# Performance work log

Measured on AMD Instinct MI355X. Metric: run time of the kernel, lower is better.

## Reference

```python
import jax, jax.numpy as jnp
import numpy as np

ALPHA = 0.2  # LeakyReLU negative slope


def setup_inputs() -> dict:
    key = jax.random.key(0)
    k1, k2, k3, k4 = jax.random.split(key, 4)
    B, N, F_IN, F_OUT = 4, 4096, 256, 256
    h = jax.random.normal(k1, (B, N, F_IN), dtype=jnp.float32)
    adj = jax.random.randint(k2, (B, N, N), 0, 2, dtype=jnp.int32)
    # xavier_normal with gain=1.414: std = gain*sqrt(2/(fan_in+fan_out))
    std_W = 1.414 * np.sqrt(2.0 / (F_IN + F_OUT))
    W = jax.random.normal(k3, (F_IN, F_OUT), dtype=jnp.float32) * std_W
    std_a = 1.414 * np.sqrt(2.0 / (1 + 2 * F_OUT))
    a = jax.random.normal(k4, (1, 2 * F_OUT), dtype=jnp.float32) * std_a
    return {"h": h, "adj": adj, "W": W, "a": a}


def reference(h, adj, W, a):
    # h: [B, N, F_in], adj: [B, N, N] (0/1), W: [F_in, F_out], a: [1, 2*F_out]
    F_out = W.shape[1]
    Hh = jnp.einsum('bni,io->bno', h, W)               # [B, N, F_out]
    a_src = a[0, :F_out]                                # attends to edge source i
    a_dst = a[0, F_out:]                                # attends to edge target j
    s = jnp.einsum('bno,o->bn', Hh, a_src)              # [B, N]
    d = jnp.einsum('bno,o->bn', Hh, a_dst)              # [B, N]
    # score(i,j) = a . concat(Hh_i, Hh_j) = s_i + d_j
    logits = s[:, :, None] + d[:, None, :]              # [B, N, N]
    # edge_e = exp(-leakyrelu(score)) only on edges (adj nonzero), else 0
    e = jnp.where(adj != 0,
                  jnp.exp(-jax.nn.leaky_relu(logits, negative_slope=ALPHA)),
                  jnp.zeros((), dtype=Hh.dtype))        # [B, N, N]
    rowsum = jnp.sum(e, axis=-1, keepdims=True)         # [B, N, 1]
    # rows with zero sum keep divisor 1 (as in the torch code)
    rowsum = jnp.where(rowsum == 0.0, 1.0, rowsum)
    h_prime = jnp.einsum('bnm,bmo->bno', e, Hh) / rowsum  # [B, N, F_out]
    return jax.nn.elu(h_prime)  # concat=True branch
```

## Files before the change

kernel.cpp:

```cpp
#include <hip/hip_runtime.h>

#define LRELU_ALPHA 0.2f

typedef __bf16 bf16x8 __attribute__((ext_vector_type(8)));
typedef unsigned short u16;
typedef unsigned short u16x8 __attribute__((ext_vector_type(8)));
typedef float f32x4 __attribute__((ext_vector_type(4)));
typedef int int4v __attribute__((ext_vector_type(4)));
typedef unsigned int u32;
typedef unsigned int u32x4 __attribute__((ext_vector_type(4)));
typedef unsigned long long u64;

__device__ __forceinline__ u16 f2bf(float f) {
  unsigned int u = __float_as_uint(f);
  u += 0x7fffu + ((u >> 16) & 1u);
  return (u16)(u >> 16);
}

__global__ __launch_bounds__(256) void packw(const int* __restrict__ adj,
                                             u32* __restrict__ maskg,
                                             const float* __restrict__ W,
                                             u16* __restrict__ WbT) {
  const int tid = threadIdx.x;
  if (blockIdx.x >= 4096) {
    int idx = (blockIdx.x - 4096) * 256 + tid;
    WbT[idx] = f2bf(W[(idx & 255) * 256 + (idx >> 8)]);
    return;
  }
  const int l = tid & 63, w = tid >> 6;
  const size_t row = (size_t)blockIdx.x * 4 + w;
  const int* arow = adj + row * 4096;
  u64* mrow = (u64*)(maskg + row * 128);
  for (int it = 0; it < 16; ++it) {
    const int* base = arow + it * 256;
    int v0 = base[l], v1 = base[l + 64], v2 = base[l + 128], v3 = base[l + 192];
    u64 b0 = __ballot(v0 != 0);
    u64 b1 = __ballot(v1 != 0);
    u64 b2 = __ballot(v2 != 0);
    u64 b3 = __ballot(v3 != 0);
    if (l == 0) {
      mrow[it * 4 + 0] = b0;
      mrow[it * 4 + 1] = b1;
      mrow[it * 4 + 2] = b2;
      mrow[it * 4 + 3] = b3;
    }
  }
}

__global__ __launch_bounds__(256) void gemm1(const float* __restrict__ h,
                                             const u16* __restrict__ WbT,
                                             const float* __restrict__ a,
                                             u16* __restrict__ HhTt,
                                             float* __restrict__ sbuf,
                                             float* __restrict__ dbuf) {
  const int tid = threadIdx.x, bid = blockIdx.x;
  const int l = tid & 63, w = tid >> 6;
  const int lr = l & 15;
  const int lk = (l >> 4) << 3;
  const int rowA = bid * 64 + 16 * w + lr;
  const float* hrow = h + (size_t)rowA * 256 + lk;

  f32x4 acc[16];
#pragma unroll
  for (int n = 0; n < 16; ++n) acc[n] = (f32x4){0.f, 0.f, 0.f, 0.f};

  for (int k0 = 0; k0 < 256; k0 += 32) {
    f32x4 a0 = *(const f32x4*)(hrow + k0);
    f32x4 a1 = *(const f32x4*)(hrow + k0 + 4);
    u16x8 au;
    au[0] = f2bf(a0[0]); au[1] = f2bf(a0[1]); au[2] = f2bf(a0[2]); au[3] = f2bf(a0[3]);
    au[4] = f2bf(a1[0]); au[5] = f2bf(a1[1]); au[6] = f2bf(a1[2]); au[7] = f2bf(a1[3]);
    bf16x8 af = __builtin_bit_cast(bf16x8, au);
#pragma unroll
    for (int n = 0; n < 16; ++n) {
      int4v bv = *(const int4v*)(WbT + (size_t)(16 * n + lr) * 256 + k0 + lk);
      bf16x8 bf = __builtin_bit_cast(bf16x8, bv);
      acc[n] = __builtin_amdgcn_mfma_f32_16x16x32_bf16(af, bf, acc[n], 0, 0, 0);
    }
  }

  float sp[4] = {0.f, 0.f, 0.f, 0.f}, dp[4] = {0.f, 0.f, 0.f, 0.f};
#pragma unroll
  for (int n = 0; n < 16; ++n) {
    int col = 16 * n + lr;
    float as = a[col];
    float ad = a[256 + col];
#pragma unroll
    for (int rr = 0; rr < 4; ++rr) {
      int row = bid * 64 + 16 * w + ((l >> 4) << 2) + rr;
      int bb = row >> 12, kk = row & 4095;
      float v = acc[n][rr];
      size_t addr = (size_t)bb * 1048576 + (size_t)(kk >> 5) * 8192 +
                    (col >> 4) * 512 + ((kk >> 3) & 3) * 128 + (col & 15) * 8 +
                    (kk & 7);
      HhTt[addr] = f2bf(v);
      sp[rr] += v * as;
      dp[rr] += v * ad;
    }
  }
#pragma unroll
  for (int rr = 0; rr < 4; ++rr) {
#pragma unroll
    for (int off = 1; off < 16; off <<= 1) {
      sp[rr] += __shfl_xor(sp[rr], off);
      dp[rr] += __shfl_xor(dp[rr], off);
    }
  }
  if ((l & 15) == 0) {
#pragma unroll
    for (int rr = 0; rr < 4; ++rr) {
      int row = bid * 64 + 16 * w + ((l >> 4) << 2) + rr;
      sbuf[row] = sp[rr];
      dbuf[row] = dp[rr];
    }
  }
}

__global__ __launch_bounds__(256, 2) void gat_main(const u32* __restrict__ maskg,
                                                   const u16* __restrict__ HhTt,
                                                   const float* __restrict__ s,
                                                   const float* __restrict__ d,
                                                   float* __restrict__ out) {
  __shared__ __align__(16) u32 Mk[32 * 128];
  __shared__ __align__(16) float Dl[4096];

  const int tid = threadIdx.x, bid = blockIdx.x;
  const int xcd = bid & 7;
  const int t = (xcd << 6) | (bid >> 3);
  const int b = t >> 7;
  const int rowbase = (t & 127) << 5;

  const int l = tid & 63, w = tid >> 6;
  const int lr = l & 15, lkg = l >> 4;
  const int wr = w & 1, wc = w >> 1;
  const int rowl = wr * 16 + lr;

  for (int i = tid; i < 1024; i += 256)
    *(f32x4*)&Dl[i * 4] = *(const f32x4*)(d + b * 4096 + i * 4);
  {
    const u32* mrow = maskg + ((size_t)(b * 4096 + rowbase)) * 128;
    const int r = tid >> 3, c0 = (tid & 7) * 16;
#pragma unroll
    for (int j = 0; j < 16; ++j) {
      int c = c0 + j;
      Mk[r * 128 + ((c + r) & 127)] = mrow[r * 128 + c];
    }
  }
  const float s_row = s[b * 4096 + rowbase + rowl];
  __syncthreads();

  const char* bsrc = (const char*)HhTt +
      ((size_t)b * 1048576 + (wc * 8) * 512 + lkg * 128 + lr * 8) * 2;

  f32x4 acc[8];
#pragma unroll
  for (int n = 0; n < 8; ++n) acc[n] = (f32x4){0.f, 0.f, 0.f, 0.f};
  float racc = 0.f;
  const int mkbase = rowl * 128;

  for (int step = 0; step < 128; ++step) {
    const char* bs = bsrc + (size_t)step * 16384;
    int4v bv[8];
#pragma unroll
    for (int n = 0; n < 8; ++n) bv[n] = *(const int4v*)(bs + n * 1024);

    u32 mword = Mk[mkbase + ((step + rowl) & 127)];
    u32 m8 = mword >> (lkg * 8);
    f32x4 dA = *(const f32x4*)&Dl[step * 32 + lkg * 8];
    f32x4 dB = *(const f32x4*)&Dl[step * 32 + lkg * 8 + 4];
    float ev[8];
#pragma unroll
    for (int j = 0; j < 8; ++j) {
      float lg = s_row + (j < 4 ? dA[j & 3] : dB[j & 3]);
      float tt = fmaxf(lg, LRELU_ALPHA * lg);
      float e = ((m8 >> j) & 1) ? __expf(-tt) : 0.f;
      racc += e;
      ev[j] = e;
    }
    u32x4 pk;
    asm("v_cvt_pk_bf16_f32 %0, %1, %2" : "=v"(pk[0]) : "v"(ev[0]), "v"(ev[1]));
    asm("v_cvt_pk_bf16_f32 %0, %1, %2" : "=v"(pk[1]) : "v"(ev[2]), "v"(ev[3]));
    asm("v_cvt_pk_bf16_f32 %0, %1, %2" : "=v"(pk[2]) : "v"(ev[4]), "v"(ev[5]));
    asm("v_cvt_pk_bf16_f32 %0, %1, %2" : "=v"(pk[3]) : "v"(ev[6]), "v"(ev[7]));
    bf16x8 af = __builtin_bit_cast(bf16x8, pk);

#pragma unroll
    for (int n = 0; n < 8; ++n) {
      bf16x8 bfv = __builtin_bit_cast(bf16x8, bv[n]);
      acc[n] = __builtin_amdgcn_mfma_f32_16x16x32_bf16(af, bfv, acc[n], 0, 0, 0);
    }
  }

  racc += __shfl_xor(racc, 16);
  racc += __shfl_xor(racc, 32);
  float inv[4];
#pragma unroll
  for (int reg = 0; reg < 4; ++reg) {
    float rsv = __shfl(racc, lkg * 4 + reg);
    inv[reg] = 1.f / (rsv == 0.f ? 1.f : rsv);
  }

  const size_t obase =
      ((size_t)(b * 4096 + rowbase + wr * 16 + lkg * 4)) * 256 + wc * 128;
#pragma unroll
  for (int n = 0; n < 8; ++n) {
#pragma unroll
    for (int reg = 0; reg < 4; ++reg) {
      float v = acc[n][reg] * inv[reg];
      out[obase + (size_t)reg * 256 + 16 * n + lr] =
          v > 0.f ? v : (__expf(v) - 1.f);
    }
  }
}

extern "C" void kernel_launch(void* const* d_in, const int* in_sizes, int n_in,
                              void* d_out, int out_size, void* d_ws, size_t ws_size,
                              hipStream_t stream) {
  const float* h = (const float*)d_in[0];
  const int* adj = (const int*)d_in[1];
  const float* W = (const float*)d_in[2];
  const float* a = (const float*)d_in[3];
  float* out = (float*)d_out;

  u16* WbT   = (u16*)d_ws;
  u16* HhTt  = (u16*)((char*)d_ws + 131072);
  float* sb  = (float*)((char*)d_ws + 131072 + 8388608);
  float* db  = sb + 16384;
  u32* maskg = (u32*)((char*)d_ws + 131072 + 8388608 + 131072);

  hipLaunchKernelGGL(packw,    dim3(4352), dim3(256), 0, stream, adj, maskg, W, WbT);
  hipLaunchKernelGGL(gemm1,    dim3(256),  dim3(256), 0, stream, h, WbT, a, HhTt, sb, db);
  hipLaunchKernelGGL(gat_main, dim3(512),  dim3(256), 0, stream, maskg, HhTt, sb, db, out);
}
```

Measured before the change: 172.0 us.

## Split gat_main output columns across blocks, double-buffer loads, raise MFMA priority

Reorganises gat_main into 512-thread blocks that each cover 64 rows and half of the output features, giving every wave 4 MFMA tiles instead of 8. The step loop is software-pipelined with two register buffers, so the next step's B-fragment, mask word and d values are loaded while the current step computes. The MFMA group is wrapped in s_setprio to raise its issue priority. In exchange, each row's exp/mask work is now recomputed by four waves instead of two. The launch bound of 512 threads with 4 blocks caps registers tightly and may cause spills, and LDS per block grows to 48KB, which limits how many blocks fit on a CU.

```diff
diff --git a/kernel.cpp b/kernel.cpp
--- a/kernel.cpp
+++ b/kernel.cpp
@@ -116,26 +116,28 @@
   }
 }
 
-__global__ __launch_bounds__(256, 2) void gat_main(const u32* __restrict__ maskg,
+__global__ __launch_bounds__(512, 4) void gat_main(const u32* __restrict__ maskg,
                                                    const u16* __restrict__ HhTt,
                                                    const float* __restrict__ s,
                                                    const float* __restrict__ d,
                                                    float* __restrict__ out) {
-  __shared__ __align__(16) u32 Mk[32 * 128];
+  __shared__ __align__(16) u32 Mk[64 * 128];
   __shared__ __align__(16) float Dl[4096];
 
   const int tid = threadIdx.x, bid = blockIdx.x;
   const int xcd = bid & 7;
   const int t = (xcd << 6) | (bid >> 3);
   const int b = t >> 7;
-  const int rowbase = (t & 127) << 5;
+  const int loc = t & 127;
+  const int rowbase = (loc >> 1) << 6;
+  const int ch = loc & 1;
 
   const int l = tid & 63, w = tid >> 6;
   const int lr = l & 15, lkg = l >> 4;
-  const int wr = w & 1, wc = w >> 1;
+  const int wr = w & 3, wc = w >> 2;
   const int rowl = wr * 16 + lr;
 
-  for (int i = tid; i < 1024; i += 256)
+  for (int i = tid; i < 1024; i += 512)
     *(f32x4*)&Dl[i * 4] = *(const f32x4*)(d + b * 4096 + i * 4);
   {
     const u32* mrow = maskg + ((size_t)(b * 4096 + rowbase)) * 128;
@@ -150,46 +152,70 @@
   __syncthreads();
 
   const char* bsrc = (const char*)HhTt +
-      ((size_t)b * 1048576 + (wc * 8) * 512 + lkg * 128 + lr * 8) * 2;
-
-  f32x4 acc[8];
-#pragma unroll
-  for (int n = 0; n < 8; ++n) acc[n] = (f32x4){0.f, 0.f, 0.f, 0.f};
+      ((size_t)b * 1048576 + (size_t)(ch * 8 + wc * 4) * 512 + lkg * 128 + lr * 8) * 2;
+
+  f32x4 acc[4];
+#pragma unroll
+  for (int n = 0; n < 4; ++n) acc[n] = (f32x4){0.f, 0.f, 0.f, 0.f};
   float racc = 0.f;
   const int mkbase = rowl * 128;
 
-  for (int step = 0; step < 128; ++step) {
-    const char* bs = bsrc + (size_t)step * 16384;
-    int4v bv[8];
-#pragma unroll
-    for (int n = 0; n < 8; ++n) bv[n] = *(const int4v*)(bs + n * 1024);
-
-    u32 mword = Mk[mkbase + ((step + rowl) & 127)];
-    u32 m8 = mword >> (lkg * 8);
-    f32x4 dA = *(const f32x4*)&Dl[step * 32 + lkg * 8];
-    f32x4 dB = *(const f32x4*)&Dl[step * 32 + lkg * 8 + 4];
-    float ev[8];
-#pragma unroll
-    for (int j = 0; j < 8; ++j) {
-      float lg = s_row + (j < 4 ? dA[j & 3] : dB[j & 3]);
-      float tt = fmaxf(lg, LRELU_ALPHA * lg);
-      float e = ((m8 >> j) & 1) ? __expf(-tt) : 0.f;
-      racc += e;
-      ev[j] = e;
-    }
-    u32x4 pk;
-    asm("v_cvt_pk_bf16_f32 %0, %1, %2" : "=v"(pk[0]) : "v"(ev[0]), "v"(ev[1]));
-    asm("v_cvt_pk_bf16_f32 %0, %1, %2" : "=v"(pk[1]) : "v"(ev[2]), "v"(ev[3]));
-    asm("v_cvt_pk_bf16_f32 %0, %1, %2" : "=v"(pk[2]) : "v"(ev[4]), "v"(ev[5]));
-    asm("v_cvt_pk_bf16_f32 %0, %1, %2" : "=v"(pk[3]) : "v"(ev[6]), "v"(ev[7]));
-    bf16x8 af = __builtin_bit_cast(bf16x8, pk);
-
-#pragma unroll
-    for (int n = 0; n < 8; ++n) {
-      bf16x8 bfv = __builtin_bit_cast(bf16x8, bv[n]);
-      acc[n] = __builtin_amdgcn_mfma_f32_16x16x32_bf16(af, bfv, acc[n], 0, 0, 0);
-    }
-  }
+  int4v bvA0, bvA1, bvA2, bvA3, bvB0, bvB1, bvB2, bvB3;
+  u32 mwA, mwB;
+  f32x4 dA0, dA1, dB0, dB1;
+
+#define LOADSTEP(S, STEP)                                                     \
+  {                                                                           \
+    const int st_ = (STEP) & 127;                                             \
+    const char* bs_ = bsrc + (size_t)st_ * 16384;                             \
+    bv##S##0 = *(const int4v*)(bs_);                                          \
+    bv##S##1 = *(const int4v*)(bs_ + 1024);                                   \
+    bv##S##2 = *(const int4v*)(bs_ + 2048);                                   \
+    bv##S##3 = *(const int4v*)(bs_ + 3072);                                   \
+    mw##S = Mk[mkbase + ((st_ + rowl) & 127)];                                \
+    d##S##0 = *(const f32x4*)&Dl[st_ * 32 + lkg * 8];                         \
+    d##S##1 = *(const f32x4*)&Dl[st_ * 32 + lkg * 8 + 4];                     \
+  }
+
+#define COMP(S)                                                               \
+  {                                                                           \
+    u32 m8 = mw##S >> (lkg * 8);                                              \
+    float ev[8];                                                              \
+    _Pragma("unroll")                                                         \
+    for (int j = 0; j < 8; ++j) {                                             \
+      float lg = s_row + (j < 4 ? d##S##0[j & 3] : d##S##1[j & 3]);           \
+      float tt = fmaxf(lg, LRELU_ALPHA * lg);                                 \
+      float e = ((m8 >> j) & 1) ? __expf(-tt) : 0.f;                          \
+      racc += e;                                                              \
+      ev[j] = e;                                                              \
+    }                                                                         \
+    u32x4 pk;                                                                 \
+    asm("v_cvt_pk_bf16_f32 %0, %1, %2" : "=v"(pk[0]) : "v"(ev[0]), "v"(ev[1])); \
+    asm("v_cvt_pk_bf16_f32 %0, %1, %2" : "=v"(pk[1]) : "v"(ev[2]), "v"(ev[3])); \
+    asm("v_cvt_pk_bf16_f32 %0, %1, %2" : "=v"(pk[2]) : "v"(ev[4]), "v"(ev[5])); \
+    asm("v_cvt_pk_bf16_f32 %0, %1, %2" : "=v"(pk[3]) : "v"(ev[6]), "v"(ev[7])); \
+    bf16x8 af = __builtin_bit_cast(bf16x8, pk);                               \
+    __builtin_amdgcn_s_setprio(1);                                            \
+    acc[0] = __builtin_amdgcn_mfma_f32_16x16x32_bf16(                         \
+        af, __builtin_bit_cast(bf16x8, bv##S##0), acc[0], 0, 0, 0);           \
+    acc[1] = __builtin_amdgcn_mfma_f32_16x16x32_bf16(                         \
+        af, __builtin_bit_cast(bf16x8, bv##S##1), acc[1], 0, 0, 0);           \
+    acc[2] = __builtin_amdgcn_mfma_f32_16x16x32_bf16(                         \
+        af, __builtin_bit_cast(bf16x8, bv##S##2), acc[2], 0, 0, 0);           \
+    acc[3] = __builtin_amdgcn_mfma_f32_16x16x32_bf16(                         \
+        af, __builtin_bit_cast(bf16x8, bv##S##3), acc[3], 0, 0, 0);           \
+    __builtin_amdgcn_s_setprio(0);                                            \
+  }
+
+  LOADSTEP(A, 0)
+  for (int st = 0; st < 128; st += 2) {
+    LOADSTEP(B, st + 1)
+    COMP(A)
+    LOADSTEP(A, st + 2)
+    COMP(B)
+  }
+#undef LOADSTEP
+#undef COMP
 
   racc += __shfl_xor(racc, 16);
   racc += __shfl_xor(racc, 32);
@@ -201,9 +227,9 @@
   }
 
   const size_t obase =
-      ((size_t)(b * 4096 + rowbase + wr * 16 + lkg * 4)) * 256 + wc * 128;
-#pragma unroll
-  for (int n = 0; n < 8; ++n) {
+      ((size_t)(b * 4096 + rowbase + wr * 16 + lkg * 4)) * 256 + ch * 128 + wc * 64;
+#pragma unroll
+  for (int n = 0; n < 4; ++n) {
 #pragma unroll
     for (int reg = 0; reg < 4; ++reg) {
       float v = acc[n][reg] * inv[reg];
@@ -230,5 +256,5 @@
 
   hipLaunchKernelGGL(packw,    dim3(4352), dim3(256), 0, stream, adj, maskg, W, WbT);
   hipLaunchKernelGGL(gemm1,    dim3(256),  dim3(256), 0, stream, h, WbT, a, HhTt, sb, db);
-  hipLaunchKernelGGL(gat_main, dim3(512),  dim3(256), 0, stream, maskg, HhTt, sb, db, out);
-}
+  hipLaunchKernelGGL(gat_main, dim3(512),  dim3(512), 0, stream, maskg, HhTt, sb, db, out);
+}
```

Result: slower. 176.1 us (+2.4%).

## Fuse adjacency bit-packing into main kernel and switch to 32x32 MFMA tiles

Applied to the files above, without the earlier changes.

Removes the separate packing pass that wrote a bitmask to global memory. The main attention kernel now reads the int32 adjacency directly and ballots it into a shared-memory bitmask per block. Blocks grow to 512 threads covering 64 rows each, and the inner loop uses 32x32x16 bf16 MFMAs with a matching new Hh layout and s_setprio around the MFMA group. This avoids a global round trip for the mask and improves MFMA reuse, but adjacency reads are no longer overlapped with other work and the block count halves.

```diff
diff --git a/kernel.cpp b/kernel.cpp
--- a/kernel.cpp
+++ b/kernel.cpp
@@ -6,6 +6,7 @@
 typedef unsigned short u16;
 typedef unsigned short u16x8 __attribute__((ext_vector_type(8)));
 typedef float f32x4 __attribute__((ext_vector_type(4)));
+typedef float f32x16 __attribute__((ext_vector_type(16)));
 typedef int int4v __attribute__((ext_vector_type(4)));
 typedef unsigned int u32;
 typedef unsigned int u32x4 __attribute__((ext_vector_type(4)));
@@ -17,34 +18,10 @@
   return (u16)(u >> 16);
 }
 
-__global__ __launch_bounds__(256) void packw(const int* __restrict__ adj,
-                                             u32* __restrict__ maskg,
-                                             const float* __restrict__ W,
+__global__ __launch_bounds__(256) void wcast(const float* __restrict__ W,
                                              u16* __restrict__ WbT) {
-  const int tid = threadIdx.x;
-  if (blockIdx.x >= 4096) {
-    int idx = (blockIdx.x - 4096) * 256 + tid;
-    WbT[idx] = f2bf(W[(idx & 255) * 256 + (idx >> 8)]);
-    return;
-  }
-  const int l = tid & 63, w = tid >> 6;
-  const size_t row = (size_t)blockIdx.x * 4 + w;
-  const int* arow = adj + row * 4096;
-  u64* mrow = (u64*)(maskg + row * 128);
-  for (int it = 0; it < 16; ++it) {
-    const int* base = arow + it * 256;
-    int v0 = base[l], v1 = base[l + 64], v2 = base[l + 128], v3 = base[l + 192];
-    u64 b0 = __ballot(v0 != 0);
-    u64 b1 = __ballot(v1 != 0);
-    u64 b2 = __ballot(v2 != 0);
-    u64 b3 = __ballot(v3 != 0);
-    if (l == 0) {
-      mrow[it * 4 + 0] = b0;
-      mrow[it * 4 + 1] = b1;
-      mrow[it * 4 + 2] = b2;
-      mrow[it * 4 + 3] = b3;
-    }
-  }
+  int idx = blockIdx.x * 256 + threadIdx.x;
+  WbT[idx] = f2bf(W[(idx & 255) * 256 + (idx >> 8)]);
 }
 
 __global__ __launch_bounds__(256) void gemm1(const float* __restrict__ h,
@@ -90,9 +67,8 @@
       int row = bid * 64 + 16 * w + ((l >> 4) << 2) + rr;
       int bb = row >> 12, kk = row & 4095;
       float v = acc[n][rr];
-      size_t addr = (size_t)bb * 1048576 + (size_t)(kk >> 5) * 8192 +
-                    (col >> 4) * 512 + ((kk >> 3) & 3) * 128 + (col & 15) * 8 +
-                    (kk & 7);
+      size_t addr = (size_t)bb * 1048576 + (size_t)(kk >> 4) * 4096 +
+                    (col >> 5) * 512 + (col & 31) * 16 + (kk & 15);
       HhTt[addr] = f2bf(v);
       sp[rr] += v * as;
       dp[rr] += v * ad;
@@ -116,100 +92,125 @@
   }
 }
 
-__global__ __launch_bounds__(256, 2) void gat_main(const u32* __restrict__ maskg,
-                                                   const u16* __restrict__ HhTt,
-                                                   const float* __restrict__ s,
-                                                   const float* __restrict__ d,
-                                                   float* __restrict__ out) {
-  __shared__ __align__(16) u32 Mk[32 * 128];
+__global__ __launch_bounds__(512, 2) void gat_fused(const int* __restrict__ adj,
+                                                    const u16* __restrict__ HhTt,
+                                                    const float* __restrict__ s,
+                                                    const float* __restrict__ d,
+                                                    float* __restrict__ out) {
+  __shared__ __align__(16) u32 Mk[64 * 128];
   __shared__ __align__(16) float Dl[4096];
 
   const int tid = threadIdx.x, bid = blockIdx.x;
   const int xcd = bid & 7;
-  const int t = (xcd << 6) | (bid >> 3);
-  const int b = t >> 7;
-  const int rowbase = (t & 127) << 5;
+  const int t = (xcd << 5) | (bid >> 3);
+  const int b = t >> 6;
+  const int rowbase = (t & 63) << 6;
 
   const int l = tid & 63, w = tid >> 6;
-  const int lr = l & 15, lkg = l >> 4;
   const int wr = w & 1, wc = w >> 1;
-  const int rowl = wr * 16 + lr;
-
-  for (int i = tid; i < 1024; i += 256)
+  const int lc = l & 31, kh8 = l >> 5;
+  const int rowloc = wr * 32 + lc;
+
+  for (int i = tid; i < 1024; i += 512)
     *(f32x4*)&Dl[i * 4] = *(const f32x4*)(d + b * 4096 + i * 4);
-  {
-    const u32* mrow = maskg + ((size_t)(b * 4096 + rowbase)) * 128;
-    const int r = tid >> 3, c0 = (tid & 7) * 16;
-#pragma unroll
-    for (int j = 0; j < 16; ++j) {
-      int c = c0 + j;
-      Mk[r * 128 + ((c + r) & 127)] = mrow[r * 128 + c];
-    }
-  }
-  const float s_row = s[b * 4096 + rowbase + rowl];
+
+  for (int rr = 0; rr < 8; ++rr) {
+    const int rloc = w * 8 + rr;
+    const int* arow = adj + ((size_t)(b * 4096 + rowbase + rloc)) * 4096;
+#pragma unroll 4
+    for (int it = 0; it < 16; ++it) {
+      const int* bp = arow + it * 256;
+      u64 b0 = __ballot(bp[l] != 0);
+      u64 b1 = __ballot(bp[l + 64] != 0);
+      u64 b2 = __ballot(bp[l + 128] != 0);
+      u64 b3 = __ballot(bp[l + 192] != 0);
+      if (l < 8) {
+        u64 sA = (l & 4) ? b2 : b0;
+        u64 sB = (l & 4) ? b3 : b1;
+        u64 sel = (l & 2) ? sB : sA;
+        u32 w32 = (u32)(sel >> ((l & 1) * 32));
+        int c = it * 8 + l;
+        Mk[rloc * 128 + ((c + rloc) & 127)] = w32;
+      }
+    }
+  }
   __syncthreads();
 
-  const char* bsrc = (const char*)HhTt +
-      ((size_t)b * 1048576 + (wc * 8) * 512 + lkg * 128 + lr * 8) * 2;
-
-  f32x4 acc[8];
-#pragma unroll
-  for (int n = 0; n < 8; ++n) acc[n] = (f32x4){0.f, 0.f, 0.f, 0.f};
+  const float s_row = s[b * 4096 + rowbase + rowloc];
+
+  const char* bbase = (const char*)HhTt + (size_t)b * 2097152 + wc * 2048 +
+                      lc * 32 + kh8 * 16;
+
+  f32x16 acc0 = {0.f}, acc1 = {0.f};
+#pragma unroll
+  for (int i = 0; i < 16; ++i) { acc0[i] = 0.f; acc1[i] = 0.f; }
   float racc = 0.f;
-  const int mkbase = rowl * 128;
-
-  for (int step = 0; step < 128; ++step) {
-    const char* bs = bsrc + (size_t)step * 16384;
-    int4v bv[8];
-#pragma unroll
-    for (int n = 0; n < 8; ++n) bv[n] = *(const int4v*)(bs + n * 1024);
-
-    u32 mword = Mk[mkbase + ((step + rowl) & 127)];
-    u32 m8 = mword >> (lkg * 8);
-    f32x4 dA = *(const f32x4*)&Dl[step * 32 + lkg * 8];
-    f32x4 dB = *(const f32x4*)&Dl[step * 32 + lkg * 8 + 4];
-    float ev[8];
+  const int mkb = rowloc * 128;
+
+  for (int st = 0; st < 128; ++st) {
+    const char* bs = bbase + (size_t)st * 16384;
+    int4v b00 = *(const int4v*)(bs);
+    int4v b01 = *(const int4v*)(bs + 1024);
+    int4v b10 = *(const int4v*)(bs + 8192);
+    int4v b11 = *(const int4v*)(bs + 9216);
+
+    u32 mword = Mk[mkb + ((st + rowloc) & 127)];
+    f32x4 d0 = *(const f32x4*)&Dl[st * 32 + kh8 * 8];
+    f32x4 d1 = *(const f32x4*)&Dl[st * 32 + kh8 * 8 + 4];
+    f32x4 d2 = *(const f32x4*)&Dl[st * 32 + 16 + kh8 * 8];
+    f32x4 d3 = *(const f32x4*)&Dl[st * 32 + 20 + kh8 * 8];
+
+    u32 m0 = mword >> (kh8 * 8);
+    u32 m1 = mword >> (16 + kh8 * 8);
+    float e0[8], e1[8];
 #pragma unroll
     for (int j = 0; j < 8; ++j) {
-      float lg = s_row + (j < 4 ? dA[j & 3] : dB[j & 3]);
-      float tt = fmaxf(lg, LRELU_ALPHA * lg);
-      float e = ((m8 >> j) & 1) ? __expf(-tt) : 0.f;
-      racc += e;
-      ev[j] = e;
-    }
-    u32x4 pk;
-    asm("v_cvt_pk_bf16_f32 %0, %1, %2" : "=v"(pk[0]) : "v"(ev[0]), "v"(ev[1]));
-    asm("v_cvt_pk_bf16_f32 %0, %1, %2" : "=v"(pk[1]) : "v"(ev[2]), "v"(ev[3]));
-    asm("v_cvt_pk_bf16_f32 %0, %1, %2" : "=v"(pk[2]) : "v"(ev[4]), "v"(ev[5]));
-    asm("v_cvt_pk_bf16_f32 %0, %1, %2" : "=v"(pk[3]) : "v"(ev[6]), "v"(ev[7]));
-    bf16x8 af = __builtin_bit_cast(bf16x8, pk);
-
-#pragma unroll
-    for (int n = 0; n < 8; ++n) {
-      bf16x8 bfv = __builtin_bit_cast(bf16x8, bv[n]);
-      acc[n] = __builtin_amdgcn_mfma_f32_16x16x32_bf16(af, bfv, acc[n], 0, 0, 0);
-    }
-  }
-
-  racc += __shfl_xor(racc, 16);
+      float lgA = s_row + (j < 4 ? d0[j & 3] : d1[j & 3]);
+      float tA = fmaxf(lgA, LRELU_ALPHA * lgA);
+      float eA = ((m0 >> j) & 1) ? __expf(-tA) : 0.f;
+      float lgB = s_row + (j < 4 ? d2[j & 3] : d3[j & 3]);
+      float tB = fmaxf(lgB, LRELU_ALPHA * lgB);
+      float eB = ((m1 >> j) & 1) ? __expf(-tB) : 0.f;
+      racc += eA + eB;
+      e0[j] = eA;
+      e1[j] = eB;
+    }
+    u32x4 p0, p1;
+    asm("v_cvt_pk_bf16_f32 %0, %1, %2" : "=v"(p0[0]) : "v"(e0[0]), "v"(e0[1]));
+    asm("v_cvt_pk_bf16_f32 %0, %1, %2" : "=v"(p0[1]) : "v"(e0[2]), "v"(e0[3]));
+    asm("v_cvt_pk_bf16_f32 %0, %1, %2" : "=v"(p0[2]) : "v"(e0[4]), "v"(e0[5]));
+    asm("v_cvt_pk_bf16_f32 %0, %1, %2" : "=v"(p0[3]) : "v"(e0[6]), "v"(e0[7]));
+    asm("v_cvt_pk_bf16_f32 %0, %1, %2" : "=v"(p1[0]) : "v"(e1[0]), "v"(e1[1]));
+    asm("v_cvt_pk_bf16_f32 %0, %1, %2" : "=v"(p1[1]) : "v"(e1[2]), "v"(e1[3]));
+    asm("v_cvt_pk_bf16_f32 %0, %1, %2" : "=v"(p1[2]) : "v"(e1[4]), "v"(e1[5]));
+    asm("v_cvt_pk_bf16_f32 %0, %1, %2" : "=v"(p1[3]) : "v"(e1[6]), "v"(e1[7]));
+    bf16x8 af0 = __builtin_bit_cast(bf16x8, p0);
+    bf16x8 af1 = __builtin_bit_cast(bf16x8, p1);
+
+    __builtin_amdgcn_s_setprio(1);
+    acc0 = __builtin_amdgcn_mfma_f32_32x32x16_bf16(
+        af0, __builtin_bit_cast(bf16x8, b00), acc0, 0, 0, 0);
+    acc1 = __builtin_amdgcn_mfma_f32_32x32x16_bf16(
+        af0, __builtin_bit_cast(bf16x8, b01), acc1, 0, 0, 0);
+    acc0 = __builtin_amdgcn_mfma_f32_32x32x16_bf16(
+        af1, __builtin_bit_cast(bf16x8, b10), acc0, 0, 0, 0);
+    acc1 = __builtin_amdgcn_mfma_f32_32x32x16_bf16(
+        af1, __builtin_bit_cast(bf16x8, b11), acc1, 0, 0, 0);
+    __builtin_amdgcn_s_setprio(0);
+  }
+
   racc += __shfl_xor(racc, 32);
-  float inv[4];
-#pragma unroll
-  for (int reg = 0; reg < 4; ++reg) {
-    float rsv = __shfl(racc, lkg * 4 + reg);
-    inv[reg] = 1.f / (rsv == 0.f ? 1.f : rsv);
-  }
-
-  const size_t obase =
-      ((size_t)(b * 4096 + rowbase + wr * 16 + lkg * 4)) * 256 + wc * 128;
-#pragma unroll
-  for (int n = 0; n < 8; ++n) {
-#pragma unroll
-    for (int reg = 0; reg < 4; ++reg) {
-      float v = acc[n][reg] * inv[reg];
-      out[obase + (size_t)reg * 256 + 16 * n + lr] =
-          v > 0.f ? v : (__expf(v) - 1.f);
-    }
+
+#pragma unroll
+  for (int reg = 0; reg < 16; ++reg) {
+    const int rl = (reg & 3) + 8 * (reg >> 2) + 4 * kh8;
+    float rsv = __shfl(racc, rl);
+    float inv = 1.f / (rsv == 0.f ? 1.f : rsv);
+    const size_t grow = (size_t)(b * 4096 + rowbase + wr * 32 + rl);
+    float v0 = acc0[reg] * inv;
+    float v1 = acc1[reg] * inv;
+    out[grow * 256 + wc * 64 + lc] = v0 > 0.f ? v0 : (__expf(v0) - 1.f);
+    out[grow * 256 + wc * 64 + 32 + lc] = v1 > 0.f ? v1 : (__expf(v1) - 1.f);
   }
 }
 
@@ -222,13 +223,12 @@
   const float* a = (const float*)d_in[3];
   float* out = (float*)d_out;
 
-  u16* WbT   = (u16*)d_ws;
-  u16* HhTt  = (u16*)((char*)d_ws + 131072);
-  float* sb  = (float*)((char*)d_ws + 131072 + 8388608);
-  float* db  = sb + 16384;
-  u32* maskg = (u32*)((char*)d_ws + 131072 + 8388608 + 131072);
-
-  hipLaunchKernelGGL(packw,    dim3(4352), dim3(256), 0, stream, adj, maskg, W, WbT);
-  hipLaunchKernelGGL(gemm1,    dim3(256),  dim3(256), 0, stream, h, WbT, a, HhTt, sb, db);
-  hipLaunchKernelGGL(gat_main, dim3(512),  dim3(256), 0, stream, maskg, HhTt, sb, db, out);
-}
+  u16* WbT  = (u16*)d_ws;
+  u16* HhTt = (u16*)((char*)d_ws + 131072);
+  float* sb = (float*)((char*)d_ws + 131072 + 8388608);
+  float* db = sb + 16384;
+
+  hipLaunchKernelGGL(wcast,     dim3(256), dim3(256), 0, stream, W, WbT);
+  hipLaunchKernelGGL(gemm1,     dim3(256), dim3(256), 0, stream, h, WbT, a, HhTt, sb, db);
+  hipLaunchKernelGGL(gat_fused, dim3(256), dim3(512), 0, stream, adj, HhTt, sb, db, out);
+}
```

Result: slower. 210.4 us (+22.3%).

## Share edge-weight tiles via LDS across 16 waves and merge mask pack with gemm

Applied to the files above, without the earlier changes.

The main attention kernel now uses 1024-thread blocks covering 64 rows. Each thread computes only two exp values per step and writes them into a 4-deep LDS ring of bf16 A tiles. Each wave loads one B fragment per step, with the next one register-prefetched, and runs MFMAs against all four 16-row tiles. This cuts redundant exp work and raises reuse of the B operand, at the cost of a block barrier every step. Separately, the adjacency bit-packing and the Hh gemm are fused into a single launch so they run concurrently, and the W cast moves to its own small kernel.

```diff
diff --git a/kernel.cpp b/kernel.cpp
--- a/kernel.cpp
+++ b/kernel.cpp
@@ -8,7 +8,6 @@
 typedef float f32x4 __attribute__((ext_vector_type(4)));
 typedef int int4v __attribute__((ext_vector_type(4)));
 typedef unsigned int u32;
-typedef unsigned int u32x4 __attribute__((ext_vector_type(4)));
 typedef unsigned long long u64;
 
 __device__ __forceinline__ u16 f2bf(float f) {
@@ -17,44 +16,45 @@
   return (u16)(u >> 16);
 }
 
-__global__ __launch_bounds__(256) void packw(const int* __restrict__ adj,
-                                             u32* __restrict__ maskg,
-                                             const float* __restrict__ W,
+__global__ __launch_bounds__(256) void wcast(const float* __restrict__ W,
                                              u16* __restrict__ WbT) {
+  int idx = blockIdx.x * 256 + threadIdx.x;
+  WbT[idx] = f2bf(W[(idx & 255) * 256 + (idx >> 8)]);
+}
+
+__global__ __launch_bounds__(256) void packgemm(const int* __restrict__ adj,
+                                                u32* __restrict__ maskg,
+                                                const float* __restrict__ h,
+                                                const u16* __restrict__ WbT,
+                                                const float* __restrict__ a,
+                                                u16* __restrict__ HhTt,
+                                                float* __restrict__ sbuf,
+                                                float* __restrict__ dbuf) {
   const int tid = threadIdx.x;
-  if (blockIdx.x >= 4096) {
-    int idx = (blockIdx.x - 4096) * 256 + tid;
-    WbT[idx] = f2bf(W[(idx & 255) * 256 + (idx >> 8)]);
+  const int l = tid & 63, w = tid >> 6;
+
+  if (blockIdx.x >= 256) {
+    const size_t row = (size_t)(blockIdx.x - 256) * 4 + w;
+    const int* arow = adj + row * 4096;
+    u64* mrow = (u64*)(maskg + row * 128);
+    for (int it = 0; it < 16; ++it) {
+      const int* base = arow + it * 256;
+      int v0 = base[l], v1 = base[l + 64], v2 = base[l + 128], v3 = base[l + 192];
+      u64 b0 = __ballot(v0 != 0);
+      u64 b1 = __ballot(v1 != 0);
+      u64 b2 = __ballot(v2 != 0);
+      u64 b3 = __ballot(v3 != 0);
+      if (l == 0) {
+        mrow[it * 4 + 0] = b0;
+        mrow[it * 4 + 1] = b1;
+        mrow[it * 4 + 2] = b2;
+        mrow[it * 4 + 3] = b3;
+      }
+    }
     return;
   }
-  const int l = tid & 63, w = tid >> 6;
-  const size_t row = (size_t)blockIdx.x * 4 + w;
-  const int* arow = adj + row * 4096;
-  u64* mrow = (u64*)(maskg + row * 128);
-  for (int it = 0; it < 16; ++it) {
-    const int* base = arow + it * 256;
-    int v0 = base[l], v1 = base[l + 64], v2 = base[l + 128], v3 = base[l + 192];
-    u64 b0 = __ballot(v0 != 0);
-    u64 b1 = __ballot(v1 != 0);
-    u64 b2 = __ballot(v2 != 0);
-    u64 b3 = __ballot(v3 != 0);
-    if (l == 0) {
-      mrow[it * 4 + 0] = b0;
-      mrow[it * 4 + 1] = b1;
-      mrow[it * 4 + 2] = b2;
-      mrow[it * 4 + 3] = b3;
-    }
-  }
-}
-
-__global__ __launch_bounds__(256) void gemm1(const float* __restrict__ h,
-                                             const u16* __restrict__ WbT,
-                                             const float* __restrict__ a,
-                                             u16* __restrict__ HhTt,
-                                             float* __restrict__ sbuf,
-                                             float* __restrict__ dbuf) {
-  const int tid = threadIdx.x, bid = blockIdx.x;
-  const int l = tid & 63, w = tid >> 6;
+
+  const int bid = blockIdx.x;
   const int lr = l & 15;
   const int lk = (l >> 4) << 3;
   const int rowA = bid * 64 + 16 * w + lr;
@@ -116,98 +116,110 @@
   }
 }
 
-__global__ __launch_bounds__(256, 2) void gat_main(const u32* __restrict__ maskg,
-                                                   const u16* __restrict__ HhTt,
-                                                   const float* __restrict__ s,
-                                                   const float* __restrict__ d,
-                                                   float* __restrict__ out) {
-  __shared__ __align__(16) u32 Mk[32 * 128];
-  __shared__ __align__(16) float Dl[4096];
+__global__ __launch_bounds__(1024, 4) void gat_main(const u32* __restrict__ maskg,
+                                                    const u16* __restrict__ HhTt,
+                                                    const float* __restrict__ s,
+                                                    const float* __restrict__ d,
+                                                    float* __restrict__ out) {
+  __shared__ __align__(16) u32 Mk[64 * 128];
+  __shared__ __align__(16) u16 At[4][2560];
+  __shared__ float rs_lds[64];
 
   const int tid = threadIdx.x, bid = blockIdx.x;
   const int xcd = bid & 7;
-  const int t = (xcd << 6) | (bid >> 3);
-  const int b = t >> 7;
-  const int rowbase = (t & 127) << 5;
+  const int t = (xcd << 5) | (bid >> 3);
+  const int b = t >> 6;
+  const int rowbase = (t & 63) << 6;
 
   const int l = tid & 63, w = tid >> 6;
   const int lr = l & 15, lkg = l >> 4;
-  const int wr = w & 1, wc = w >> 1;
-  const int rowl = wr * 16 + lr;
-
-  for (int i = tid; i < 1024; i += 256)
-    *(f32x4*)&Dl[i * 4] = *(const f32x4*)(d + b * 4096 + i * 4);
+  const int r = tid >> 4, kp = tid & 15;
+
   {
     const u32* mrow = maskg + ((size_t)(b * 4096 + rowbase)) * 128;
-    const int r = tid >> 3, c0 = (tid & 7) * 16;
-#pragma unroll
-    for (int j = 0; j < 16; ++j) {
+    const int c0 = kp * 8;
+#pragma unroll
+    for (int j = 0; j < 8; ++j) {
       int c = c0 + j;
       Mk[r * 128 + ((c + r) & 127)] = mrow[r * 128 + c];
     }
   }
-  const float s_row = s[b * 4096 + rowbase + rowl];
+  const float s_r = s[b * 4096 + rowbase + r];
+  const float* dtp = d + b * 4096 + kp * 2;
+
+  float racc = 0.f;
+
+#define EGEN(BUF, STE)                                                        \
+  {                                                                           \
+    u32 mword = Mk[r * 128 + (((STE) + r) & 127)];                            \
+    u32 mb = mword >> (kp * 2);                                               \
+    float2 dv = *(const float2*)(dtp + (STE) * 32);                           \
+    float lg0 = s_r + dv.x;                                                   \
+    float t0 = fmaxf(lg0, LRELU_ALPHA * lg0);                                 \
+    float e0 = (mb & 1u) ? __expf(-t0) : 0.f;                                 \
+    float lg1 = s_r + dv.y;                                                   \
+    float t1 = fmaxf(lg1, LRELU_ALPHA * lg1);                                 \
+    float e1 = (mb & 2u) ? __expf(-t1) : 0.f;                                 \
+    racc += e0 + e1;                                                          \
+    u32 pk;                                                                   \
+    asm("v_cvt_pk_bf16_f32 %0, %1, %2" : "=v"(pk) : "v"(e0), "v"(e1));        \
+    *(u32*)&At[BUF][r * 40 + kp * 2] = pk;                                    \
+  }
+
   __syncthreads();
-
-  const char* bsrc = (const char*)HhTt +
-      ((size_t)b * 1048576 + (wc * 8) * 512 + lkg * 128 + lr * 8) * 2;
-
-  f32x4 acc[8];
-#pragma unroll
-  for (int n = 0; n < 8; ++n) acc[n] = (f32x4){0.f, 0.f, 0.f, 0.f};
-  float racc = 0.f;
-  const int mkbase = rowl * 128;
-
-  for (int step = 0; step < 128; ++step) {
-    const char* bs = bsrc + (size_t)step * 16384;
-    int4v bv[8];
-#pragma unroll
-    for (int n = 0; n < 8; ++n) bv[n] = *(const int4v*)(bs + n * 1024);
-
-    u32 mword = Mk[mkbase + ((step + rowl) & 127)];
-    u32 m8 = mword >> (lkg * 8);
-    f32x4 dA = *(const f32x4*)&Dl[step * 32 + lkg * 8];
-    f32x4 dB = *(const f32x4*)&Dl[step * 32 + lkg * 8 + 4];
-    float ev[8];
-#pragma unroll
-    for (int j = 0; j < 8; ++j) {
-      float lg = s_row + (j < 4 ? dA[j & 3] : dB[j & 3]);
-      float tt = fmaxf(lg, LRELU_ALPHA * lg);
-      float e = ((m8 >> j) & 1) ? __expf(-tt) : 0.f;
-      racc += e;
-      ev[j] = e;
-    }
-    u32x4 pk;
-    asm("v_cvt_pk_bf16_f32 %0, %1, %2" : "=v"(pk[0]) : "v"(ev[0]), "v"(ev[1]));
-    asm("v_cvt_pk_bf16_f32 %0, %1, %2" : "=v"(pk[1]) : "v"(ev[2]), "v"(ev[3]));
-    asm("v_cvt_pk_bf16_f32 %0, %1, %2" : "=v"(pk[2]) : "v"(ev[4]), "v"(ev[5]));
-    asm("v_cvt_pk_bf16_f32 %0, %1, %2" : "=v"(pk[3]) : "v"(ev[6]), "v"(ev[7]));
-    bf16x8 af = __builtin_bit_cast(bf16x8, pk);
-
-#pragma unroll
-    for (int n = 0; n < 8; ++n) {
-      bf16x8 bfv = __builtin_bit_cast(bf16x8, bv[n]);
-      acc[n] = __builtin_amdgcn_mfma_f32_16x16x32_bf16(af, bfv, acc[n], 0, 0, 0);
-    }
-  }
-
-  racc += __shfl_xor(racc, 16);
-  racc += __shfl_xor(racc, 32);
-  float inv[4];
-#pragma unroll
-  for (int reg = 0; reg < 4; ++reg) {
-    float rsv = __shfl(racc, lkg * 4 + reg);
-    inv[reg] = 1.f / (rsv == 0.f ? 1.f : rsv);
-  }
-
-  const size_t obase =
-      ((size_t)(b * 4096 + rowbase + wr * 16 + lkg * 4)) * 256 + wc * 128;
-#pragma unroll
-  for (int n = 0; n < 8; ++n) {
+  EGEN(0, 0)
+
+  const char* bbase = (const char*)HhTt + (size_t)b * 2097152 + w * 1024 + l * 16;
+  int4v Bcur = *(const int4v*)(bbase);
+
+  f32x4 acc[4];
+#pragma unroll
+  for (int n = 0; n < 4; ++n) acc[n] = (f32x4){0.f, 0.f, 0.f, 0.f};
+
+  for (int st = 0; st < 128; ++st) {
+    if (st < 127) EGEN((st + 1) & 3, st + 1)
+    const int pst = (st < 127) ? st + 1 : st;
+    int4v Bnext = *(const int4v*)(bbase + (size_t)pst * 16384);
+
+    asm volatile("s_waitcnt lgkmcnt(0)" ::: "memory");
+    __builtin_amdgcn_s_barrier();
+    __builtin_amdgcn_sched_barrier(0);
+
+    const u16* atb = &At[st & 3][0];
+    int4v a0 = *(const int4v*)(atb + (0 * 16 + lr) * 40 + lkg * 8);
+    int4v a1 = *(const int4v*)(atb + (1 * 16 + lr) * 40 + lkg * 8);
+    int4v a2 = *(const int4v*)(atb + (2 * 16 + lr) * 40 + lkg * 8);
+    int4v a3 = *(const int4v*)(atb + (3 * 16 + lr) * 40 + lkg * 8);
+    bf16x8 bfv = __builtin_bit_cast(bf16x8, Bcur);
+    __builtin_amdgcn_s_setprio(1);
+    acc[0] = __builtin_amdgcn_mfma_f32_16x16x32_bf16(
+        __builtin_bit_cast(bf16x8, a0), bfv, acc[0], 0, 0, 0);
+    acc[1] = __builtin_amdgcn_mfma_f32_16x16x32_bf16(
+        __builtin_bit_cast(bf16x8, a1), bfv, acc[1], 0, 0, 0);
+    acc[2] = __builtin_amdgcn_mfma_f32_16x16x32_bf16(
+        __builtin_bit_cast(bf16x8, a2), bfv, acc[2], 0, 0, 0);
+    acc[3] = __builtin_amdgcn_mfma_f32_16x16x32_bf16(
+        __builtin_bit_cast(bf16x8, a3), bfv, acc[3], 0, 0, 0);
+    __builtin_amdgcn_s_setprio(0);
+    Bcur = Bnext;
+  }
+#undef EGEN
+
+  racc += __shfl_xor(racc, 1);
+  racc += __shfl_xor(racc, 2);
+  racc += __shfl_xor(racc, 4);
+  racc += __shfl_xor(racc, 8);
+  if (kp == 0) rs_lds[r] = (racc == 0.f) ? 1.f : racc;
+  __syncthreads();
+
+#pragma unroll
+  for (int rt = 0; rt < 4; ++rt) {
 #pragma unroll
     for (int reg = 0; reg < 4; ++reg) {
-      float v = acc[n][reg] * inv[reg];
-      out[obase + (size_t)reg * 256 + 16 * n + lr] =
+      int rloc = rt * 16 + lkg * 4 + reg;
+      float rsv = rs_lds[rloc];
+      float v = acc[rt][reg] / rsv;
+      out[((size_t)(b * 4096 + rowbase + rloc)) * 256 + w * 16 + lr] =
           v > 0.f ? v : (__expf(v) - 1.f);
     }
   }
@@ -228,7 +240,9 @@
   float* db  = sb + 16384;
   u32* maskg = (u32*)((char*)d_ws + 131072 + 8388608 + 131072);
 
-  hipLaunchKernelGGL(packw,    dim3(4352), dim3(256), 0, stream, adj, maskg, W, WbT);
-  hipLaunchKernelGGL(gemm1,    dim3(256),  dim3(256), 0, stream, h, WbT, a, HhTt, sb, db);
-  hipLaunchKernelGGL(gat_main, dim3(512),  dim3(256), 0, stream, maskg, HhTt, sb, db, out);
-}
+  hipLaunchKernelGGL(wcast,    dim3(256),  dim3(256),  0, stream, W, WbT);
+  hipLaunchKernelGGL(packgemm, dim3(4352), dim3(256),  0, stream,
+                     adj, maskg, h, WbT, a, HhTt, sb, db);
+  hipLaunchKernelGGL(gat_main, dim3(256),  dim3(1024), 0, stream,
+                     maskg, HhTt, sb, db, out);
+}
```

Result: slower. 180.6 us (+5.0%).
